# Optimization experiments

Measured on AMD Instinct MI355X. Metric: run time of the kernel, lower is better.

Reference implementation:

```python
import jax, jax.numpy as jnp
import numpy as np

D_MODEL = 1024
N_HEADS = 16
HEAD_DIM = D_MODEL // N_HEADS


def setup_inputs() -> dict:
    key = jax.random.key(0)
    ks = jax.random.split(key, 9)
    s = 1.0 / np.sqrt(D_MODEL)
    x = jax.random.normal(ks[0], (2, 2048, D_MODEL), dtype=jnp.float32)
    Wq = jax.random.uniform(ks[1], (D_MODEL, D_MODEL), jnp.float32, -s, s)
    bq = jax.random.uniform(ks[2], (D_MODEL,), jnp.float32, -s, s)
    Wk = jax.random.uniform(ks[3], (D_MODEL, D_MODEL), jnp.float32, -s, s)
    bk = jax.random.uniform(ks[4], (D_MODEL,), jnp.float32, -s, s)
    Wv = jax.random.uniform(ks[5], (D_MODEL, D_MODEL), jnp.float32, -s, s)
    bv = jax.random.uniform(ks[6], (D_MODEL,), jnp.float32, -s, s)
    Wo = jax.random.uniform(ks[7], (D_MODEL, D_MODEL), jnp.float32, -s, s)
    bo = jax.random.uniform(ks[8], (D_MODEL,), jnp.float32, -s, s)
    return {"x": x, "Wq": Wq, "bq": bq, "Wk": Wk, "bk": bk,
            "Wv": Wv, "bv": bv, "Wo": Wo, "bo": bo}


def reference(x, Wq, bq, Wk, bk, Wv, bv, Wo, bo):
    B, S, _ = x.shape
    # project and split heads: [B, H, S, Dh]
    def heads(W, b):
        return (x @ W + b).reshape(B, S, N_HEADS, HEAD_DIM).transpose(0, 2, 1, 3)
    Q, K, V = heads(Wq, bq), heads(Wk, bk), heads(Wv, bv)
    scale = 1.0 / np.sqrt(HEAD_DIM).astype(np.float32)
    scores = jnp.einsum('bhsd,bhtd->bhst', Q, K) * scale  # [B,H,S,S]
    causal = jnp.tril(jnp.ones((S, S), dtype=bool))
    scores = jnp.where(causal, scores, -jnp.inf)
    attn = jax.nn.softmax(scores, axis=-1)
    out = jnp.einsum('bhst,bhtd->bhsd', attn, V)  # [B,H,S,Dh]
    out = out.transpose(0, 2, 1, 3).reshape(B, S, D_MODEL)
    return out @ Wo + bo
```

## Files before the change

### kernel.cpp

```cpp
#include <hip/hip_runtime.h>

typedef __attribute__((ext_vector_type(8))) __bf16 bfrag;
typedef __attribute__((ext_vector_type(4))) float f32x4;

#define MFMA(a, b, c) __builtin_amdgcn_mfma_f32_16x16x32_bf16((a), (b), (c), 0, 0, 0)

#define D_MODEL 1024
#define SEQ     2048
#define NB      2
#define NH      16
#define HD      64
#define MROWS   (NB * SEQ)

#define SCALE_LOG2 0.18033688011112043f
#define NEG_BIG    (-3.0e38f)

#define GLOBAL_AS(p) ((const __attribute__((address_space(1))) void*)(p))
#define LDS_AS(p)    ((__attribute__((address_space(3))) void*)(p))
#define ASYNC_CP16(g, l) __builtin_amdgcn_global_load_lds(GLOBAL_AS(g), LDS_AS(l), 16, 0, 0)

__global__ __launch_bounds__(256) void k_prep(
    const float* __restrict__ x,
    const float* __restrict__ Wq, const float* __restrict__ Wk,
    const float* __restrict__ Wv, const float* __restrict__ Wo,
    __bf16* __restrict__ Wt, __bf16* __restrict__ xb)
{
    __shared__ __bf16 t[64][65];
    if (blockIdx.z == 4) {
        size_t base = ((size_t)(blockIdx.y * 16 + blockIdx.x)) * 16384;
        for (int j = 0; j < 8; ++j) {
            size_t i = base + (size_t)j * 2048 + (size_t)threadIdx.x * 8;
            float4 f0 = *(const float4*)&x[i];
            float4 f1 = *(const float4*)&x[i + 4];
            union { uint4 u; __bf16 h[8]; } cv;
            cv.h[0] = (__bf16)f0.x; cv.h[1] = (__bf16)f0.y;
            cv.h[2] = (__bf16)f0.z; cv.h[3] = (__bf16)f0.w;
            cv.h[4] = (__bf16)f1.x; cv.h[5] = (__bf16)f1.y;
            cv.h[6] = (__bf16)f1.z; cv.h[7] = (__bf16)f1.w;
            *(uint4*)&xb[i] = cv.u;
        }
        return;
    }
    const float* src = (blockIdx.z == 0) ? Wq : (blockIdx.z == 1) ? Wk
                      : (blockIdx.z == 2) ? Wv : Wo;
    __bf16* dst = Wt + (size_t)blockIdx.z * (1024u * 1024u);
    int tr = blockIdx.y * 64, tc = blockIdx.x * 64;
    for (int j = 0; j < 16; ++j) {
        int id = threadIdx.x + j * 256;
        int r = id >> 6, c = id & 63;
        t[r][c] = (__bf16)src[(size_t)(tr + r) * 1024 + tc + c];
    }
    __syncthreads();
    for (int j = 0; j < 2; ++j) {
        int id = threadIdx.x + j * 256;
        int r = id >> 3;
        int c8 = (id & 7) * 8;
        union { uint4 u; __bf16 h[8]; } pk;
        for (int i = 0; i < 8; ++i) pk.h[i] = t[c8 + i][r];
        *(uint4*)&dst[(size_t)(tc + r) * 1024 + tr + c8] = pk.u;
    }
}

template <int MODE, bool WT>
__global__ __launch_bounds__(256) void k_gemm128(
    const void* __restrict__ Ap,
    const void* __restrict__ W0, const void* __restrict__ W1,
    const void* __restrict__ W2,
    const float* __restrict__ b0, const float* __restrict__ b1,
    const float* __restrict__ b2, void* __restrict__ dstp)
{
    constexpr int AST = WT ? 64 : 72;
    alignas(16) __shared__ __bf16 SH[18432];
    __bf16* As = SH;
    __bf16* Bs = SH + 128 * AST;

    const int tid = threadIdx.x;
    const int z = blockIdx.z;
    const int m0 = blockIdx.y * 128;
    const int n0 = blockIdx.x * 128;
    const void* W     = (z == 0) ? W0 : (z == 1) ? W1 : W2;
    const float* bias = (z == 0) ? b0 : (z == 1) ? b1 : b2;

    const int wid = tid >> 6, lane = tid & 63;
    const int quad = lane >> 4, l16 = lane & 15;
    const int wRow = (wid >> 1) * 64, wCol = (wid & 1) * 64;

    f32x4 acc[4][4];
    const f32x4 zero = {0.f, 0.f, 0.f, 0.f};
    for (int mi = 0; mi < 4; ++mi)
        for (int ni = 0; ni < 4; ++ni) acc[mi][ni] = zero;

    const int srow = tid >> 3;
    const int sseg = (tid & 7) * 8;
    const int bkrow = tid >> 4;
    const int bnseg = (tid & 15) * 8;
    const int arow = lane >> 3;
    const int akoff = ((lane & 7) * 8) ^ (arow * 8);
    const int sw = (l16 & 7) * 8;

    for (int k0 = 0; k0 < D_MODEL; k0 += 64) {
        __syncthreads();
        if (WT) {
            const __bf16* Ab = (const __bf16*)Ap;
            const __bf16* Bt = (const __bf16*)W;
            for (int it = 0; it < 4; ++it) {
                int row = wid * 32 + it * 8;
                ASYNC_CP16(&Ab[(size_t)(m0 + row + arow) * D_MODEL + k0 + akoff],
                           &As[row * 64]);
                ASYNC_CP16(&Bt[(size_t)(n0 + row + arow) * D_MODEL + k0 + akoff],
                           &Bs[row * 64]);
            }
        } else {
            if (MODE == 0) {
                const float* A = (const float*)Ap;
                for (int it = 0; it < 4; ++it) {
                    int row = srow + it * 32;
                    const float* src = &A[(size_t)(m0 + row) * D_MODEL + k0 + sseg];
                    float4 f0 = *(const float4*)src;
                    float4 f1 = *(const float4*)(src + 4);
                    union { uint4 u; __bf16 h[8]; } cv;
                    cv.h[0] = (__bf16)f0.x; cv.h[1] = (__bf16)f0.y;
                    cv.h[2] = (__bf16)f0.z; cv.h[3] = (__bf16)f0.w;
                    cv.h[4] = (__bf16)f1.x; cv.h[5] = (__bf16)f1.y;
                    cv.h[6] = (__bf16)f1.z; cv.h[7] = (__bf16)f1.w;
                    *(uint4*)&As[row * AST + sseg] = cv.u;
                }
            } else {
                const __bf16* A = (const __bf16*)Ap;
                for (int it = 0; it < 4; ++it) {
                    int row = srow + it * 32;
                    uint4 va = *(const uint4*)&A[(size_t)(m0 + row) * D_MODEL + k0 + sseg];
                    *(uint4*)&As[row * AST + sseg] = va;
                }
            }
            const float* Wf = (const float*)W;
            for (int it = 0; it < 4; ++it) {
                int krow = bkrow + it * 16;
                const float* src = &Wf[(size_t)(k0 + krow) * D_MODEL + n0 + bnseg];
                float4 f0 = *(const float4*)src;
                float4 f1 = *(const float4*)(src + 4);
                Bs[(bnseg + 0) * AST + krow] = (__bf16)f0.x;
                Bs[(bnseg + 1) * AST + krow] = (__bf16)f0.y;
                Bs[(bnseg + 2) * AST + krow] = (__bf16)f0.z;
                Bs[(bnseg + 3) * AST + krow] = (__bf16)f0.w;
                Bs[(bnseg + 4) * AST + krow] = (__bf16)f1.x;
                Bs[(bnseg + 5) * AST + krow] = (__bf16)f1.y;
                Bs[(bnseg + 6) * AST + krow] = (__bf16)f1.z;
                Bs[(bnseg + 7) * AST + krow] = (__bf16)f1.w;
            }
        }
        __syncthreads();
        for (int kk = 0; kk < 64; kk += 32) {
            bfrag af[4], bf[4];
            if (WT) {
                int ko = (kk + quad * 8) ^ sw;
                for (int mi = 0; mi < 4; ++mi)
                    af[mi] = *(const bfrag*)&As[(wRow + mi * 16 + l16) * 64 + ko];
                for (int ni = 0; ni < 4; ++ni)
                    bf[ni] = *(const bfrag*)&Bs[(wCol + ni * 16 + l16) * 64 + ko];
            } else {
                for (int mi = 0; mi < 4; ++mi)
                    af[mi] = *(const bfrag*)&As[(wRow + mi * 16 + l16) * AST + kk + quad * 8];
                for (int ni = 0; ni < 4; ++ni)
                    bf[ni] = *(const bfrag*)&Bs[(wCol + ni * 16 + l16) * AST + kk + quad * 8];
            }
            for (int mi = 0; mi < 4; ++mi)
                for (int ni = 0; ni < 4; ++ni)
                    acc[mi][ni] = MFMA(af[mi], bf[ni], acc[mi][ni]);
        }
    }

    if (MODE == 0) {
        float biasv[4];
        for (int ni = 0; ni < 4; ++ni) biasv[ni] = bias[n0 + wCol + ni * 16 + l16];
        const int b = m0 >> 11, m0s = m0 & 2047, h0 = n0 >> 6;
        __syncthreads();
        if (z < 2) {
            for (int mi = 0; mi < 4; ++mi)
                for (int ni = 0; ni < 4; ++ni) {
                    int col = wCol + ni * 16 + l16;
                    for (int r = 0; r < 4; ++r) {
                        float v = acc[mi][ni][r] + biasv[ni];
                        if (z == 0) v *= SCALE_LOG2;
                        SH[(wRow + mi * 16 + quad * 4 + r) * 136 + col] = (__bf16)v;
                    }
                }
            __syncthreads();
            __bf16* qk = (__bf16*)dstp + (size_t)z * (MROWS * (size_t)D_MODEL);
            for (int i = 0; i < 8; ++i) {
                int rid = i * 32 + (tid >> 3);
                int hl = rid >> 7, sl = rid & 127;
                int dcol = (tid & 7) * 8;
                uint4 v = *(const uint4*)&SH[sl * 136 + hl * 64 + dcol];
                *(uint4*)&qk[(((size_t)b * NH + h0 + hl) * SEQ + m0s + sl) * HD + dcol] = v;
            }
        } else {
            for (int mi = 0; mi < 4; ++mi)
                for (int ni = 0; ni < 4; ++ni) {
                    int col = wCol + ni * 16 + l16;
                    int s0 = wRow + mi * 16 + quad * 4;
                    union { unsigned long long u; __bf16 h4[4]; } pk;
                    for (int r = 0; r < 4; ++r)
                        pk.h4[r] = (__bf16)(acc[mi][ni][r] + biasv[ni]);
                    *(unsigned long long*)&SH[col * 136 + s0] = pk.u;
                }
            __syncthreads();
            __bf16* vv = (__bf16*)dstp + (size_t)2 * (MROWS * (size_t)D_MODEL);
            for (int i = 0; i < 8; ++i) {
                int rid = i * 16 + (tid >> 4);
                int hl = rid >> 6, d = rid & 63;
                int sc = (tid & 15) * 8;
                uint4 v = *(const uint4*)&SH[rid * 136 + sc];
                *(uint4*)&vv[(((size_t)b * NH + h0 + hl) * HD + d) * SEQ + m0s + sc] = v;
            }
        }
    } else {
        for (int mi = 0; mi < 4; ++mi)
            for (int ni = 0; ni < 4; ++ni) {
                int gn = n0 + wCol + ni * 16 + l16;
                float bv = bias[gn];
                for (int r = 0; r < 4; ++r) {
                    int gm = m0 + wRow + mi * 16 + quad * 4 + r;
                    ((float*)dstp)[(size_t)gm * D_MODEL + gn] = acc[mi][ni][r] + bv;
                }
            }
    }
}

__global__ __launch_bounds__(256) void k_gemm_out(
    const __bf16* __restrict__ A, const __bf16* __restrict__ Bt,
    const float* __restrict__ bias, float* __restrict__ dst)
{
    alignas(16) __shared__ __bf16 As[64 * 64];
    alignas(16) __shared__ __bf16 Bs[128 * 64];

    const int tid = threadIdx.x;
    const int m0 = blockIdx.y * 64;
    const int n0 = blockIdx.x * 128;
    const int wid = tid >> 6, lane = tid & 63;
    const int quad = lane >> 4, l16 = lane & 15;
    const int wRow = (wid >> 1) * 32, wCol = (wid & 1) * 64;

    f32x4 acc[2][4];
    const f32x4 zero = {0.f, 0.f, 0.f, 0.f};
    for (int mi = 0; mi < 2; ++mi)
        for (int ni = 0; ni < 4; ++ni) acc[mi][ni] = zero;

    const int arow = lane >> 3;
    const int akoff = ((lane & 7) * 8) ^ (arow * 8);
    const int sw = (l16 & 7) * 8;

    for (int k0 = 0; k0 < D_MODEL; k0 += 64) {
        __syncthreads();
        for (int it = 0; it < 2; ++it) {
            int row = wid * 16 + it * 8;
            ASYNC_CP16(&A[(size_t)(m0 + row + arow) * D_MODEL + k0 + akoff],
                       &As[row * 64]);
        }
        for (int it = 0; it < 4; ++it) {
            int row = wid * 32 + it * 8;
            ASYNC_CP16(&Bt[(size_t)(n0 + row + arow) * D_MODEL + k0 + akoff],
                       &Bs[row * 64]);
        }
        __syncthreads();
        for (int kk = 0; kk < 64; kk += 32) {
            int ko = (kk + quad * 8) ^ sw;
            bfrag af[2], bf[4];
            for (int mi = 0; mi < 2; ++mi)
                af[mi] = *(const bfrag*)&As[(wRow + mi * 16 + l16) * 64 + ko];
            for (int ni = 0; ni < 4; ++ni)
                bf[ni] = *(const bfrag*)&Bs[(wCol + ni * 16 + l16) * 64 + ko];
            for (int mi = 0; mi < 2; ++mi)
                for (int ni = 0; ni < 4; ++ni)
                    acc[mi][ni] = MFMA(af[mi], bf[ni], acc[mi][ni]);
        }
    }

    for (int mi = 0; mi < 2; ++mi)
        for (int ni = 0; ni < 4; ++ni) {
            int gn = n0 + wCol + ni * 16 + l16;
            float bv = bias[gn];
            for (int r = 0; r < 4; ++r) {
                int gm = m0 + wRow + mi * 16 + quad * 4 + r;
                dst[(size_t)gm * D_MODEL + gn] = acc[mi][ni][r] + bv;
            }
        }
}

template <bool SPLIT>
__global__ __launch_bounds__(256) void k_attn(
    const __bf16* __restrict__ Q, const __bf16* __restrict__ K,
    const __bf16* __restrict__ Vt, __bf16* __restrict__ O,
    float* __restrict__ Po, float* __restrict__ Pl)
{
    alignas(16) __shared__ __bf16 Ks[64 * 64];
    alignas(16) __shared__ __bf16 Vts[64 * 64];
    alignas(16) __shared__ __bf16 Ps[4][16 * 64];

    const int tid = threadIdx.x, wid = tid >> 6, lane = tid & 63;
    const int quad = lane >> 4, l16 = lane & 15;
    const int h = blockIdx.y, b = blockIdx.z;

    int qb, t0, t1, hf = 0;
    bool partial = false;
    if (SPLIT) {
        const int xi = blockIdx.x;
        if (xi < 32) {
            qb = 31 - (xi >> 1); hf = xi & 1;
            const int n = qb + 1, nh = (n + 1) >> 1;
            t0 = hf ? nh : 0; t1 = hf ? n : nh;
            partial = true;
        } else { qb = 47 - xi; t0 = 0; t1 = qb + 1; }
    } else {
        const int u = (blockIdx.x + blockIdx.y + 16 * blockIdx.z) & 31;
        qb = (u & 1) ? 31 - (u >> 1) : (u >> 1);
        t0 = 0; t1 = qb + 1;
    }

    const size_t bh = ((size_t)b * NH + h) * SEQ * HD;
    const __bf16* Qg  = Q + bh + (size_t)qb * 64 * HD;
    const __bf16* Kg  = K + bh;
    const __bf16* Vtg = Vt + ((size_t)b * NH + h) * HD * SEQ;

    bfrag qf[2];
    qf[0] = *(const bfrag*)&Qg[(size_t)(wid * 16 + l16) * HD + quad * 8];
    qf[1] = *(const bfrag*)&Qg[(size_t)(wid * 16 + l16) * HD + 32 + quad * 8];

    const f32x4 zero = {0.f, 0.f, 0.f, 0.f};
    f32x4 o[4];
    for (int dt = 0; dt < 4; ++dt) o[dt] = zero;
    float lrow = 0.f;
    const int q = qb * 64 + wid * 16 + l16;
    const int srcbase = (lane & 48) + quad * 4;
    const int sw = (l16 & 7) * 8;

    const int row0 = tid >> 3, seg = (tid & 7) * 8;
    const int sseg = seg ^ ((row0 & 7) * 8);

    uint4 kreg0 = *(const uint4*)&Kg[(size_t)(t0 * 64 + row0) * HD + seg];
    uint4 kreg1 = *(const uint4*)&Kg[(size_t)(t0 * 64 + row0 + 32) * HD + seg];
    uint4 vreg0 = *(const uint4*)&Vtg[(size_t)row0 * SEQ + t0 * 64 + seg];
    uint4 vreg1 = *(const uint4*)&Vtg[(size_t)(row0 + 32) * SEQ + t0 * 64 + seg];

    for (int t = t0; t < t1; ++t) {
        const int j0 = t * 64;
        __syncthreads();
        *(uint4*)&Ks[row0 * 64 + sseg] = kreg0;
        *(uint4*)&Ks[(row0 + 32) * 64 + sseg] = kreg1;
        *(uint4*)&Vts[row0 * 64 + sseg] = vreg0;
        *(uint4*)&Vts[(row0 + 32) * 64 + sseg] = vreg1;
        if (t + 1 < t1) {
            const int j1 = j0 + 64;
            kreg0 = *(const uint4*)&Kg[(size_t)(j1 + row0) * HD + seg];
            kreg1 = *(const uint4*)&Kg[(size_t)(j1 + row0 + 32) * HD + seg];
            vreg0 = *(const uint4*)&Vtg[(size_t)row0 * SEQ + j1 + seg];
            vreg1 = *(const uint4*)&Vtg[(size_t)(row0 + 32) * SEQ + j1 + seg];
        }
        __syncthreads();

        f32x4 st[4];
        for (int kt = 0; kt < 4; ++kt) {
            bfrag ka0 = *(const bfrag*)&Ks[(kt * 16 + l16) * 64 + ((quad * 8) ^ sw)];
            bfrag ka1 = *(const bfrag*)&Ks[(kt * 16 + l16) * 64 + ((32 + quad * 8) ^ sw)];
            st[kt] = MFMA(ka1, qf[1], MFMA(ka0, qf[0], zero));
        }

        if (t == qb) {
            for (int kt = 0; kt < 4; ++kt)
                for (int r = 0; r < 4; ++r) {
                    float v = (j0 + kt * 16 + quad * 4 + r > q) ? NEG_BIG : st[kt][r];
                    float p = exp2f(v);
                    st[kt][r] = p;
                    lrow += p;
                }
        } else {
            for (int kt = 0; kt < 4; ++kt)
                for (int r = 0; r < 4; ++r) {
                    float p = exp2f(st[kt][r]);
                    st[kt][r] = p;
                    lrow += p;
                }
        }

        for (int kt = 0; kt < 4; ++kt) {
            union { unsigned long long u; __bf16 h4[4]; } pk;
            for (int r = 0; r < 4; ++r) pk.h4[r] = (__bf16)st[kt][r];
            *(unsigned long long*)&Ps[wid][l16 * 64 + ((kt * 16 + quad * 4) ^ sw)] = pk.u;
        }
        asm volatile("s_waitcnt lgkmcnt(0)" ::: "memory");

        for (int c = 0; c < 2; ++c) {
            int ko = (c * 32 + quad * 8) ^ sw;
            bfrag pf = *(const bfrag*)&Ps[wid][l16 * 64 + ko];
            for (int dt = 0; dt < 4; ++dt) {
                bfrag vf = *(const bfrag*)&Vts[(dt * 16 + l16) * 64 + ko];
                o[dt] = MFMA(pf, vf, o[dt]);
            }
        }
    }

    float lsum = lrow + __shfl_xor(lrow, 16, 64);
    lsum = lsum + __shfl_xor(lsum, 32, 64);

    if (!partial) {
        for (int r = 0; r < 4; ++r) {
            float lr = __shfl(lsum, srcbase + r, 64);
            float inv = 1.0f / lr;
            size_t base = ((size_t)b * SEQ + qb * 64 + wid * 16 + quad * 4 + r) * D_MODEL
                        + (size_t)h * HD;
            for (int dt = 0; dt < 4; ++dt)
                O[base + dt * 16 + l16] = (__bf16)(o[dt][r] * inv);
        }
    } else {
        const int p = (((b * NH + h) * 16) + (qb - 16)) * 2 + hf;
        float* po = Po + (size_t)p * 4096;
        for (int r = 0; r < 4; ++r) {
            int row = wid * 16 + quad * 4 + r;
            for (int dt = 0; dt < 4; ++dt)
                po[row * 64 + dt * 16 + l16] = o[dt][r];
        }
        if (quad == 0) Pl[(size_t)p * 64 + wid * 16 + l16] = lsum;
    }
}

__global__ __launch_bounds__(256) void k_attn_comb(
    const float* __restrict__ Po, const float* __restrict__ Pl,
    __bf16* __restrict__ O)
{
    const int qb = 16 + blockIdx.x, h = blockIdx.y, b = blockIdx.z;
    const int p0 = (((b * NH + h) * 16) + blockIdx.x) * 2;
    const float* o0 = Po + (size_t)p0 * 4096;
    const float* o1 = o0 + 4096;
    const int tid = threadIdx.x;
    const int row = tid >> 2, c0 = (tid & 3) * 16;
    const float inv = 1.0f / (Pl[(size_t)p0 * 64 + row] + Pl[(size_t)p0 * 64 + 64 + row]);
    union { uint4 u[2]; __bf16 hh[16]; } pk;
    for (int i = 0; i < 16; ++i)
        pk.hh[i] = (__bf16)((o0[row * 64 + c0 + i] + o1[row * 64 + c0 + i]) * inv);
    size_t base = ((size_t)b * SEQ + qb * 64 + row) * D_MODEL + (size_t)h * HD + c0;
    *(uint4*)&O[base] = pk.u[0];
    *(uint4*)&O[base + 8] = pk.u[1];
}

extern "C" void kernel_launch(void* const* d_in, const int* in_sizes, int n_in,
                              void* d_out, int out_size, void* d_ws, size_t ws_size,
                              hipStream_t stream)
{
    const float* x  = (const float*)d_in[0];
    const float* Wq = (const float*)d_in[1];
    const float* bq = (const float*)d_in[2];
    const float* Wk = (const float*)d_in[3];
    const float* bk = (const float*)d_in[4];
    const float* Wv = (const float*)d_in[5];
    const float* bv = (const float*)d_in[6];
    const float* Wo = (const float*)d_in[7];
    const float* bo = (const float*)d_in[8];

    __bf16* ws = (__bf16*)d_ws;
    const size_t M1 = 1024u * 1024u;
    __bf16* qkv    = ws;
    __bf16* attn_o = ws + 12 * M1;
    __bf16* Wt     = ws + 16 * M1;
    __bf16* xb     = ws + 20 * M1;
    float*  Po     = (float*)(ws + 24 * M1);
    float*  Pl     = (float*)(ws + 32 * M1);

    const bool fast  = ws_size >= (size_t)48 * 1024 * 1024;
    const bool split = ws_size >= (size_t)68 * 1024 * 1024;

    if (fast) {
        k_prep<<<dim3(16, 16, 5), 256, 0, stream>>>(x, Wq, Wk, Wv, Wo, Wt, xb);
        k_gemm128<0, true><<<dim3(8, 32, 3), 256, 0, stream>>>(
            xb, Wt, Wt + M1, Wt + 2 * M1, bq, bk, bv, qkv);
        if (split) {
            k_attn<true><<<dim3(48, 16, 2), 256, 0, stream>>>(
                qkv, qkv + 4 * M1, qkv + 8 * M1, attn_o, Po, Pl);
            k_attn_comb<<<dim3(16, 16, 2), 256, 0, stream>>>(Po, Pl, attn_o);
        } else {
            k_attn<false><<<dim3(32, 16, 2), 256, 0, stream>>>(
                qkv, qkv + 4 * M1, qkv + 8 * M1, attn_o, nullptr, nullptr);
        }
        k_gemm_out<<<dim3(8, 64), 256, 0, stream>>>(
            attn_o, Wt + 3 * M1, bo, (float*)d_out);
    } else {
        k_gemm128<0, false><<<dim3(8, 32, 3), 256, 0, stream>>>(
            x, Wq, Wk, Wv, bq, bk, bv, qkv);
        k_attn<false><<<dim3(32, 16, 2), 256, 0, stream>>>(
            qkv, qkv + 4 * M1, qkv + 8 * M1, attn_o, nullptr, nullptr);
        k_gemm128<1, false><<<dim3(8, 32, 1), 256, 0, stream>>>(
            attn_o, Wo, Wo, Wo, bo, bo, bo, (float*)d_out);
    }
}
```

Measured before the change: 200.8 us.

## Double-buffer K/V tiles with async global-to-LDS copies and compute row sums via MFMA

The attention kernel now loads K and V tiles straight into LDS with async global_load_lds copies into a double buffer. This replaces staging through registers and cuts one barrier per iteration. The softmax row sum is now taken by an extra MFMA of P against a ones vector rather than scalar adds and shuffles, so the sum uses the bf16-rounded probabilities. The code adds a wait on the async loads only through the barrier, so correctness relies on the compiler inserting a vmcnt wait. LDS use doubles.

```diff
diff --git a/kernel.cpp b/kernel.cpp
--- a/kernel.cpp
+++ b/kernel.cpp
@@ -293,8 +293,7 @@
     const __bf16* __restrict__ Vt, __bf16* __restrict__ O,
     float* __restrict__ Po, float* __restrict__ Pl)
 {
-    alignas(16) __shared__ __bf16 Ks[64 * 64];
-    alignas(16) __shared__ __bf16 Vts[64 * 64];
+    alignas(16) __shared__ __bf16 KVs[2][2 * 64 * 64];
     alignas(16) __shared__ __bf16 Ps[4][16 * 64];
 
     const int tid = threadIdx.x, wid = tid >> 6, lane = tid & 63;
@@ -326,37 +325,42 @@
     qf[0] = *(const bfrag*)&Qg[(size_t)(wid * 16 + l16) * HD + quad * 8];
     qf[1] = *(const bfrag*)&Qg[(size_t)(wid * 16 + l16) * HD + 32 + quad * 8];
 
+    union { uint4 u; bfrag f; } onesu;
+    onesu.u = make_uint4(0x3F803F80u, 0x3F803F80u, 0x3F803F80u, 0x3F803F80u);
+    const bfrag onesf = onesu.f;
+
     const f32x4 zero = {0.f, 0.f, 0.f, 0.f};
     f32x4 o[4];
     for (int dt = 0; dt < 4; ++dt) o[dt] = zero;
-    float lrow = 0.f;
+    f32x4 o_l = zero;
     const int q = qb * 64 + wid * 16 + l16;
-    const int srcbase = (lane & 48) + quad * 4;
     const int sw = (l16 & 7) * 8;
 
-    const int row0 = tid >> 3, seg = (tid & 7) * 8;
-    const int sseg = seg ^ ((row0 & 7) * 8);
-
-    uint4 kreg0 = *(const uint4*)&Kg[(size_t)(t0 * 64 + row0) * HD + seg];
-    uint4 kreg1 = *(const uint4*)&Kg[(size_t)(t0 * 64 + row0 + 32) * HD + seg];
-    uint4 vreg0 = *(const uint4*)&Vtg[(size_t)row0 * SEQ + t0 * 64 + seg];
-    uint4 vreg1 = *(const uint4*)&Vtg[(size_t)(row0 + 32) * SEQ + t0 * 64 + seg];
-
+    const int lr8  = lane >> 3;
+    const int aoff = ((lane & 7) * 8) ^ (lr8 * 8);
+    const int r0a = wid * 16, r0b = wid * 16 + 8;
+
+    {
+        const int j0 = t0 * 64;
+        ASYNC_CP16(&Kg[(size_t)(j0 + r0a + lr8) * HD + aoff],  &KVs[0][r0a * 64]);
+        ASYNC_CP16(&Kg[(size_t)(j0 + r0b + lr8) * HD + aoff],  &KVs[0][r0b * 64]);
+        ASYNC_CP16(&Vtg[(size_t)(r0a + lr8) * SEQ + j0 + aoff], &KVs[0][4096 + r0a * 64]);
+        ASYNC_CP16(&Vtg[(size_t)(r0b + lr8) * SEQ + j0 + aoff], &KVs[0][4096 + r0b * 64]);
+    }
+
+    int cur = 0;
     for (int t = t0; t < t1; ++t) {
+        __syncthreads();
+        if (t + 1 < t1) {
+            const int j1 = (t + 1) * 64, nb = cur ^ 1;
+            ASYNC_CP16(&Kg[(size_t)(j1 + r0a + lr8) * HD + aoff],  &KVs[nb][r0a * 64]);
+            ASYNC_CP16(&Kg[(size_t)(j1 + r0b + lr8) * HD + aoff],  &KVs[nb][r0b * 64]);
+            ASYNC_CP16(&Vtg[(size_t)(r0a + lr8) * SEQ + j1 + aoff], &KVs[nb][4096 + r0a * 64]);
+            ASYNC_CP16(&Vtg[(size_t)(r0b + lr8) * SEQ + j1 + aoff], &KVs[nb][4096 + r0b * 64]);
+        }
         const int j0 = t * 64;
-        __syncthreads();
-        *(uint4*)&Ks[row0 * 64 + sseg] = kreg0;
-        *(uint4*)&Ks[(row0 + 32) * 64 + sseg] = kreg1;
-        *(uint4*)&Vts[row0 * 64 + sseg] = vreg0;
-        *(uint4*)&Vts[(row0 + 32) * 64 + sseg] = vreg1;
-        if (t + 1 < t1) {
-            const int j1 = j0 + 64;
-            kreg0 = *(const uint4*)&Kg[(size_t)(j1 + row0) * HD + seg];
-            kreg1 = *(const uint4*)&Kg[(size_t)(j1 + row0 + 32) * HD + seg];
-            vreg0 = *(const uint4*)&Vtg[(size_t)row0 * SEQ + j1 + seg];
-            vreg1 = *(const uint4*)&Vtg[(size_t)(row0 + 32) * SEQ + j1 + seg];
-        }
-        __syncthreads();
+        const __bf16* Ks  = &KVs[cur][0];
+        const __bf16* Vts = &KVs[cur][4096];
 
         f32x4 st[4];
         for (int kt = 0; kt < 4; ++kt) {
@@ -369,17 +373,12 @@
             for (int kt = 0; kt < 4; ++kt)
                 for (int r = 0; r < 4; ++r) {
                     float v = (j0 + kt * 16 + quad * 4 + r > q) ? NEG_BIG : st[kt][r];
-                    float p = exp2f(v);
-                    st[kt][r] = p;
-                    lrow += p;
+                    st[kt][r] = exp2f(v);
                 }
         } else {
             for (int kt = 0; kt < 4; ++kt)
-                for (int r = 0; r < 4; ++r) {
-                    float p = exp2f(st[kt][r]);
-                    st[kt][r] = p;
-                    lrow += p;
-                }
+                for (int r = 0; r < 4; ++r)
+                    st[kt][r] = exp2f(st[kt][r]);
         }
 
         for (int kt = 0; kt < 4; ++kt) {
@@ -396,16 +395,14 @@
                 bfrag vf = *(const bfrag*)&Vts[(dt * 16 + l16) * 64 + ko];
                 o[dt] = MFMA(pf, vf, o[dt]);
             }
-        }
-    }
-
-    float lsum = lrow + __shfl_xor(lrow, 16, 64);
-    lsum = lsum + __shfl_xor(lsum, 32, 64);
+            o_l = MFMA(pf, onesf, o_l);
+        }
+        cur ^= 1;
+    }
 
     if (!partial) {
         for (int r = 0; r < 4; ++r) {
-            float lr = __shfl(lsum, srcbase + r, 64);
-            float inv = 1.0f / lr;
+            float inv = 1.0f / o_l[r];
             size_t base = ((size_t)b * SEQ + qb * 64 + wid * 16 + quad * 4 + r) * D_MODEL
                         + (size_t)h * HD;
             for (int dt = 0; dt < 4; ++dt)
@@ -419,7 +416,9 @@
             for (int dt = 0; dt < 4; ++dt)
                 po[row * 64 + dt * 16 + l16] = o[dt][r];
         }
-        if (quad == 0) Pl[(size_t)p * 64 + wid * 16 + l16] = lsum;
+        if (l16 == 0)
+            for (int r = 0; r < 4; ++r)
+                Pl[(size_t)p * 64 + wid * 16 + quad * 4 + r] = o_l[r];
     }
 }
 
```

Measured after the change: 205.3 us. +2.2%, slower.
